# Kernel tuning notes

Hardware: AMD Instinct MI355X
Metric: run time of the kernel (lower is better)

## Reference

```python
import jax, jax.numpy as jnp
import numpy as np

N_WORD = 50000
N_DOC = 10000
E_WW = 800000
E_WD = 320000


def _sage(h_src, h_dst, src, dst, n_dst, W_self, W_neigh, b):
    # DGL SAGEConv('mean'): fc_self(h_dst) + fc_neigh(mean_{u in N(v)} h_u) + bias
    ones = jnp.ones((src.shape[0],), dtype=h_src.dtype)
    deg = jax.ops.segment_sum(ones, dst, num_segments=n_dst)            # [n_dst]
    agg = jax.ops.segment_sum(h_src[src], dst, num_segments=n_dst)      # [n_dst, d]
    mean = agg / jnp.maximum(deg, 1.0)[:, None]                          # zero for isolated
    return h_dst @ W_self + mean @ W_neigh + b


def _layer(xw, xd, edges, Ws, Wn, b):
    (ww_s, ww_d, wwr_s, wwr_d, wd_s, wd_d, wdr_s, wdr_d) = edges
    # relations targeting 'word': word2word, word2wordr, word2documentr
    h_ww = _sage(xw, xw, ww_s, ww_d, N_WORD, Ws[0], Wn[0], b[0])
    h_wwr = _sage(xw, xw, wwr_s, wwr_d, N_WORD, Ws[1], Wn[1], b[1])
    h_wdr = _sage(xd, xw, wdr_s, wdr_d, N_WORD, Ws[3], Wn[3], b[3])
    # relation targeting 'document': word2document
    h_wd = _sage(xw, xd, wd_s, wd_d, N_DOC, Ws[2], Wn[2], b[2])
    # HeteroGraphConv aggregate='stack' then torch.sum(dim=1) == sum over relations; then relu
    return jax.nn.relu(h_ww + h_wwr + h_wdr), jax.nn.relu(h_wd)


def setup_inputs() -> dict:
    key = jax.random.key(0)
    ks = jax.random.split(key, 20)
    d_in, d_h = 256, 128
    inp = {
        "x_word": jax.random.normal(ks[0], (N_WORD, d_in), jnp.float32),
        "x_doc": jax.random.normal(ks[1], (N_DOC, d_in), jnp.float32),
        "ww_src": jax.random.randint(ks[2], (E_WW,), 0, N_WORD, jnp.int32),
        "ww_dst": jax.random.randint(ks[3], (E_WW,), 0, N_WORD, jnp.int32),
        "wwr_src": jax.random.randint(ks[4], (E_WW,), 0, N_WORD, jnp.int32),
        "wwr_dst": jax.random.randint(ks[5], (E_WW,), 0, N_WORD, jnp.int32),
        "wd_src": jax.random.randint(ks[6], (E_WD,), 0, N_WORD, jnp.int32),
        "wd_dst": jax.random.randint(ks[7], (E_WD,), 0, N_DOC, jnp.int32),
        "wdr_src": jax.random.randint(ks[8], (E_WD,), 0, N_DOC, jnp.int32),
        "wdr_dst": jax.random.randint(ks[9], (E_WD,), 0, N_WORD, jnp.int32),
        "Wself1": jax.random.normal(ks[10], (4, d_in, d_h), jnp.float32) * (1.0 / np.sqrt(d_in)),
        "Wneigh1": jax.random.normal(ks[11], (4, d_in, d_h), jnp.float32) * (1.0 / np.sqrt(d_in)),
        "b1": jnp.zeros((4, d_h), jnp.float32),
        "Wself2": jax.random.normal(ks[12], (4, d_h, d_h), jnp.float32) * (1.0 / np.sqrt(d_h)),
        "Wneigh2": jax.random.normal(ks[13], (4, d_h, d_h), jnp.float32) * (1.0 / np.sqrt(d_h)),
        "b2": jnp.zeros((4, d_h), jnp.float32),
        "lin_w": jax.random.normal(ks[14], (1, d_h), jnp.float32) * (1.0 / np.sqrt(d_h)),
        "lin_b": jnp.ones((1,), jnp.float32),
    }
    return inp


def reference(x_word, x_doc, ww_src, ww_dst, wwr_src, wwr_dst, wd_src, wd_dst,
              wdr_src, wdr_dst, Wself1, Wneigh1, b1, Wself2, Wneigh2, b2, lin_w, lin_b):
    edges = (ww_src, ww_dst, wwr_src, wwr_dst, wd_src, wd_dst, wdr_src, wdr_dst)
    xw, xd = _layer(x_word, x_doc, edges, Wself1, Wneigh1, b1)
    xw, xd = _layer(xw, xd, edges, Wself2, Wneigh2, b2)
    out_w = jax.nn.sigmoid(xw @ lin_w.T + lin_b)  # [N_WORD, 1]
    out_d = jax.nn.sigmoid(xd @ lin_w.T + lin_b)  # [N_DOC, 1]
    return out_w, out_d
```

## Files before the change

kernel.cpp:

```cpp
#include <hip/hip_runtime.h>
#include <math.h>

#define N_WORD 50000
#define N_DOC  10000
#define E_WW   800000
#define E_WD   320000
#define D_IN   256
#define D_H    128

#define NPB    1024
#define NBK_W  49
#define NBK_D  10
#define BKT    (3 * NBK_W + NBK_D)
#define EPB    4096
#define NBLK_WW 196
#define NBLK_WD 79
#define NBLK_TOT (2 * NBLK_WW + 2 * NBLK_WD)
#define PACK_BLKS 145

#define CAP_WW  18432
#define CAP_WDR 8192
#define CAP_WD  34816

#define WSTRIP ((N_WORD + 63) / 64)
#define DSTRIP ((N_DOC + 63) / 64)
#define NSTRIP (WSTRIP + DSTRIP)

typedef __attribute__((ext_vector_type(8))) short short8;
typedef __attribute__((ext_vector_type(4))) float f32x4;

__device__ inline unsigned short f2bf(float f) {
  unsigned u = __float_as_uint(f);
  u = (u + 0x7fffu + ((u >> 16) & 1u)) >> 16;
  return (unsigned short)u;
}

struct G6 { const short* B[6]; unsigned short* C[6]; };

template <int ABF, int K>
__device__ void gemm_body(const void* __restrict__ Aw, const void* __restrict__ Ad,
                          const G6& g, int blk, short* As) {
  constexpr int kd8s = (K == 256) ? 5 : 4;
  constexpr int stride = K + 8;
  constexpr int kd8 = K >> 3;
  const void* A; int M, row0, h0, h1;
  if (blk < WSTRIP) { A = Aw; M = N_WORD; row0 = blk << 6; h0 = 0; h1 = 4; }
  else { A = Ad; M = N_DOC; row0 = (blk - WSTRIP) << 6; h0 = 4; h1 = 6; }
  constexpr int total = kd8 << 6;
  for (int c = threadIdx.x; c < total; c += 256) {
    int row = c >> kd8s;
    int col8 = c & (kd8 - 1);
    int grow = row0 + row; if (grow >= M) grow = M - 1;
    short8 v;
    if (ABF) {
      v = *(const short8*)((const short*)A + (size_t)grow * K + col8 * 8);
    } else {
      const float* a = (const float*)A + (size_t)grow * K + col8 * 8;
      float4 a0 = *(const float4*)a, a1 = *(const float4*)(a + 4);
      v[0] = (short)f2bf(a0.x); v[1] = (short)f2bf(a0.y);
      v[2] = (short)f2bf(a0.z); v[3] = (short)f2bf(a0.w);
      v[4] = (short)f2bf(a1.x); v[5] = (short)f2bf(a1.y);
      v[6] = (short)f2bf(a1.z); v[7] = (short)f2bf(a1.w);
    }
    *(short8*)&As[row * stride + col8 * 8] = v;
  }
  __syncthreads();
  int wid = threadIdx.x >> 6, lane = threadIdx.x & 63;
  int r = lane & 15, quad = lane >> 4;
  constexpr int KT = K >> 5;
  int m0 = row0 + wid * 16;
  for (int h = h0; h < h1; ++h) {
    const short* Bp = g.B[h];
    f32x4 acc[8];
#pragma unroll
    for (int nt = 0; nt < 8; ++nt) acc[nt] = (f32x4){0.f, 0.f, 0.f, 0.f};
    for (int kt = 0; kt < KT; ++kt) {
      short8 af = *(const short8*)&As[(wid * 16 + r) * stride + kt * 32 + quad * 8];
      const short* bbase = Bp + ((size_t)kt * 4096) + lane * 8;
#pragma unroll
      for (int nt = 0; nt < 8; ++nt) {
        short8 bf = *(const short8*)(bbase + (size_t)nt * 512);
        acc[nt] = __builtin_amdgcn_mfma_f32_16x16x32_bf16(af, bf, acc[nt], 0, 0, 0);
      }
    }
    unsigned short* C = g.C[h];
#pragma unroll
    for (int nt = 0; nt < 8; ++nt)
#pragma unroll
      for (int rr = 0; rr < 4; ++rr) {
        int row = m0 + quad * 4 + rr;
        if (row < M) C[(size_t)row * 128 + nt * 16 + r] = f2bf(acc[nt][rr]);
      }
  }
}

struct CSRB {
  const unsigned *st_ww, *st_wwr, *st_wdr, *st_wd;
  unsigned short *c_ww, *c_wwr, *c_wdr, *c_wd;
  int *rp_ww, *rp_wwr, *rp_wdr, *rp_wd;
  const int* bcnt;
};

__device__ void place_body(int g, const CSRB& q, char* smem) {
  int* cnt = (int*)smem;
  int* off = cnt + NPB;
  int* sm  = off + NPB;
  int* s_b = sm + 256;
  const unsigned* st; unsigned short* csr; int* rp; int relFirst, relLast, n, cap, Etot;
  if (g < NBK_W)            { st = q.st_ww;  csr = q.c_ww;  rp = q.rp_ww;  relFirst = 0;         relLast = NBK_W - 1;     n = N_WORD; cap = CAP_WW;  Etot = E_WW; }
  else if (g < 2 * NBK_W)   { st = q.st_wwr; csr = q.c_wwr; rp = q.rp_wwr; relFirst = NBK_W;     relLast = 2 * NBK_W - 1; n = N_WORD; cap = CAP_WW;  Etot = E_WW; }
  else if (g < 3 * NBK_W)   { st = q.st_wdr; csr = q.c_wdr; rp = q.rp_wdr; relFirst = 2 * NBK_W; relLast = 3 * NBK_W - 1; n = N_WORD; cap = CAP_WDR; Etot = E_WD; }
  else                      { st = q.st_wd;  csr = q.c_wd;  rp = q.rp_wd;  relFirst = 3 * NBK_W; relLast = BKT - 1;       n = N_DOC;  cap = CAP_WD;  Etot = E_WD; }
  int cb = g - relFirst;
  int tid = threadIdx.x;
  if (tid < 64) {
    int v = (tid < cb) ? q.bcnt[relFirst + tid] : 0;
#pragma unroll
    for (int o = 32; o > 0; o >>= 1) v += __shfl_xor(v, o);
    if (tid == 0) s_b[0] = v;
  }
  if (g == relLast && tid == 65) rp[n] = Etot;
  int node_base = cb << 10;
  int node_cnt = n - node_base; if (node_cnt > NPB) node_cnt = NPB;
  int ecnt = q.bcnt[g];
  const unsigned* w = st + (size_t)cb * cap;
  for (int i = tid; i < NPB; i += 256) cnt[i] = 0;
  __syncthreads();
  int bstart = s_b[0];
  for (int j = tid; j < ecnt; j += 256) atomicAdd(&cnt[w[j] >> 16], 1);
  __syncthreads();
  int c[4], s = 0;
#pragma unroll
  for (int jj = 0; jj < 4; ++jj) { c[jj] = cnt[tid * 4 + jj]; s += c[jj]; }
  sm[tid] = s;
  __syncthreads();
  for (int o = 1; o < 256; o <<= 1) {
    int add = (tid >= o) ? sm[tid - o] : 0;
    __syncthreads();
    sm[tid] += add;
    __syncthreads();
  }
  int ex = sm[tid] - s;
#pragma unroll
  for (int jj = 0; jj < 4; ++jj) { off[tid * 4 + jj] = ex; ex += c[jj]; }
  __syncthreads();
#pragma unroll
  for (int jj = 0; jj < 4; ++jj) {
    int i = tid * 4 + jj;
    if (i < node_cnt) rp[node_base + i] = bstart + off[i];
  }
  __syncthreads();
  for (int j = tid; j < ecnt; j += 256) {
    unsigned e = w[j];
    int p = atomicAdd(&off[e >> 16], 1);
    csr[bstart + p] = (unsigned short)(e & 0xFFFFu);
  }
}

__global__ __launch_bounds__(256) void gemm1_place(
    const float* __restrict__ Aw, const float* __restrict__ Ad, G6 g, CSRB q) {
  __shared__ char smem[64 * 264 * 2];
  if (blockIdx.x < NSTRIP) gemm_body<0, 256>(Aw, Ad, g, blockIdx.x, (short*)smem);
  else place_body(blockIdx.x - NSTRIP, q, smem);
}

__global__ __launch_bounds__(256) void gemm2_kernel(
    const void* __restrict__ Aw, const void* __restrict__ Ad, G6 g) {
  __shared__ short As[64 * 136];
  gemm_body<1, 128>(Aw, Ad, g, blockIdx.x, As);
}

__device__ inline void rel_map(int b, const int* wwd, const int* wwrd, const int* wdrd,
                               const int* wdd, const int*& dst, int& E, int& gbase, int& lb) {
  if (b < NBLK_WW) { dst = wwd; E = E_WW; gbase = 0; lb = b; }
  else if (b < 2 * NBLK_WW) { dst = wwrd; E = E_WW; gbase = NBK_W; lb = b - NBLK_WW; }
  else if (b < 2 * NBLK_WW + NBLK_WD) { dst = wdrd; E = E_WD; gbase = 2 * NBK_W; lb = b - 2 * NBLK_WW; }
  else { dst = wdd; E = E_WD; gbase = 3 * NBK_W; lb = b - 2 * NBLK_WW - NBLK_WD; }
}

__global__ __launch_bounds__(256) void binpack_kernel(
    const int* wws, const int* wwd, const int* wwrs, const int* wwrd,
    const int* wdrs, const int* wdrd, const int* wds, const int* wdd,
    int* bcnt, unsigned* st_ww, unsigned* st_wwr, unsigned* st_wdr, unsigned* st_wd,
    const float* __restrict__ Ws1, const float* __restrict__ Wn1,
    const float* __restrict__ Ws2, const float* __restrict__ Wn2,
    short* __restrict__ Bp1, short* __restrict__ Bp2,
    const float* __restrict__ b1, const float* __restrict__ b2,
    float* __restrict__ bs1, float* __restrict__ bs2) {
  int b = blockIdx.x;
  if (b >= NBLK_TOT) {
    int tid = (b - NBLK_TOT) * 256 + threadIdx.x;
    const int L1T = 6 * 4096;
    const int L2T = 6 * 2048;
    if (tid >= L1T + L2T) {
      int t = tid - (L1T + L2T);
      if (t < 128) bs1[t] = b1[t] + b1[128 + t] + b1[384 + t];
      else if (t < 256) { int u = t - 128; bs2[u] = b2[u] + b2[128 + u] + b2[384 + u]; }
      return;
    }
    const float *src0, *src1 = nullptr, *src2 = nullptr;
    short* dstp;
    int kt, nt, lane;
    if (tid < L1T) {
      int mat = tid / 4096, rem = tid % 4096;
      kt = rem / 512; nt = (rem / 64) % 8; lane = rem % 64;
      const int W1 = 256 * 128;
      if (mat == 0) { src0 = Ws1; src1 = Ws1 + W1; src2 = Ws1 + 3 * W1; }
      else if (mat <= 4) src0 = Wn1 + (size_t)(mat - 1) * W1;
      else src0 = Ws1 + 2 * W1;
      dstp = Bp1 + (size_t)mat * W1 + ((size_t)(kt * 8 + nt) * 64 + lane) * 8;
    } else {
      int t2 = tid - L1T;
      int mat = t2 / 2048, rem = t2 % 2048;
      kt = rem / 512; nt = (rem / 64) % 8; lane = rem % 64;
      const int W2 = 128 * 128;
      if (mat == 0) { src0 = Ws2; src1 = Ws2 + W2; src2 = Ws2 + 3 * W2; }
      else if (mat <= 4) src0 = Wn2 + (size_t)(mat - 1) * W2;
      else src0 = Ws2 + 2 * W2;
      dstp = Bp2 + (size_t)mat * W2 + ((size_t)(kt * 8 + nt) * 64 + lane) * 8;
    }
    int n = nt * 16 + (lane & 15);
    int kb = kt * 32 + (lane >> 4) * 8;
    short8 v;
#pragma unroll
    for (int j = 0; j < 8; ++j) {
      float f = src0[(size_t)(kb + j) * 128 + n];
      if (src1) f += src1[(size_t)(kb + j) * 128 + n] + src2[(size_t)(kb + j) * 128 + n];
      v[j] = (short)f2bf(f);
    }
    *(short8*)dstp = v;
    return;
  }
  __shared__ int h[4][64], wb[4][64], cur[4][64];
  const int* dst; int E, gbase, lb;
  rel_map(b, wwd, wwrd, wdrd, wdd, dst, E, gbase, lb);
  const int* src; unsigned* st; int cap;
  if (b < NBLK_WW) { src = wws; st = st_ww; cap = CAP_WW; }
  else if (b < 2 * NBLK_WW) { src = wwrs; st = st_wwr; cap = CAP_WW; }
  else if (b < 2 * NBLK_WW + NBLK_WD) { src = wdrs; st = st_wdr; cap = CAP_WDR; }
  else { src = wds; st = st_wd; cap = CAP_WD; }
  int tid = threadIdx.x;
  int wave = tid >> 6;
  ((int*)h)[tid] = 0;
  ((int*)cur)[tid] = 0;
  __syncthreads();
  int e0 = lb * EPB;
#pragma unroll
  for (int k = 0; k < EPB / 256; ++k) {
    int i = e0 + k * 256 + tid;
    if (i < E) atomicAdd(&h[wave][dst[i] >> 10], 1);
  }
  __syncthreads();
  if (tid < NBK_W) {
    int t0 = h[0][tid], t1 = h[1][tid], t2 = h[2][tid], t3 = h[3][tid];
    int tot = t0 + t1 + t2 + t3;
    int base = tot ? atomicAdd(&bcnt[gbase + tid], tot) : 0;
    wb[0][tid] = base;
    wb[1][tid] = base + t0;
    wb[2][tid] = base + t0 + t1;
    wb[3][tid] = base + t0 + t1 + t2;
  }
  __syncthreads();
#pragma unroll
  for (int k = 0; k < EPB / 256; ++k) {
    int i = e0 + k * 256 + tid;
    if (i < E) {
      int d = dst[i];
      int bk = d >> 10;
      int l = atomicAdd(&cur[wave][bk], 1);
      st[(size_t)bk * cap + wb[wave][bk] + l] =
          (unsigned)(src[i] & 0xFFFF) | ((unsigned)(d & (NPB - 1)) << 16);
    }
  }
}

__device__ inline void accum_rel(const unsigned* __restrict__ y,
                                 const unsigned short* __restrict__ csr,
                                 int beg, int end, int lane, float& f0, float& f1) {
  float a0 = 0.f, a1 = 0.f;
  for (int base = beg; base < end; base += 64) {
    int cnt = end - base; if (cnt > 64) cnt = 64;
    int ld = base + lane; if (ld >= end) ld = end - 1;
    int idx = csr[ld];
    int j = 0;
    for (; j + 7 < cnt; j += 8) {
      unsigned u[8];
#pragma unroll
      for (int k = 0; k < 8; ++k) {
        int s = __builtin_amdgcn_readlane(idx, j + k);
        u[k] = y[((size_t)s << 6) + lane];
      }
#pragma unroll
      for (int k = 0; k < 8; ++k) {
        a0 += __uint_as_float(u[k] << 16);
        a1 += __uint_as_float(u[k] & 0xffff0000u);
      }
    }
    for (; j < cnt; ++j) {
      int s = __builtin_amdgcn_readlane(idx, j);
      unsigned uu = y[((size_t)s << 6) + lane];
      a0 += __uint_as_float(uu << 16);
      a1 += __uint_as_float(uu & 0xffff0000u);
    }
  }
  int deg = end - beg;
  float inv = 1.0f / (float)(deg > 1 ? deg : 1);
  f0 += a0 * inv;
  f1 += a1 * inv;
}

__global__ __launch_bounds__(256) void gather_all(
    const unsigned* __restrict__ y_ww, const unsigned* __restrict__ y_wwr,
    const unsigned* __restrict__ y_wdr, const unsigned* __restrict__ y_wd,
    const unsigned short* __restrict__ c_ww, const unsigned short* __restrict__ c_wwr,
    const unsigned short* __restrict__ c_wdr, const unsigned short* __restrict__ c_wd,
    const int* __restrict__ r_ww, const int* __restrict__ r_wwr,
    const int* __restrict__ r_wdr, const int* __restrict__ r_wd,
    const unsigned* __restrict__ tW, const unsigned* __restrict__ tD,
    const float* __restrict__ bW, const float* __restrict__ bD,
    const float* __restrict__ lw, const float* __restrict__ lb,
    unsigned* __restrict__ oW16, unsigned* __restrict__ oD16,
    float* __restrict__ oF, int mode) {
  int gn = (blockIdx.x << 2) + (threadIdx.x >> 6);
  if (gn >= N_WORD + N_DOC) return;
  int lane = threadIdx.x & 63;
  float f0, f1;
  if (gn < N_WORD) {
    int node = gn;
    unsigned tu = tW[((size_t)node << 6) + lane];
    f0 = __uint_as_float(tu << 16);
    f1 = __uint_as_float(tu & 0xffff0000u);
    accum_rel(y_ww, c_ww, r_ww[node], r_ww[node + 1], lane, f0, f1);
    accum_rel(y_wwr, c_wwr, r_wwr[node], r_wwr[node + 1], lane, f0, f1);
    accum_rel(y_wdr, c_wdr, r_wdr[node], r_wdr[node + 1], lane, f0, f1);
    float2 bv = ((const float2*)bW)[lane];
    f0 = fmaxf(f0 + bv.x, 0.f);
    f1 = fmaxf(f1 + bv.y, 0.f);
    if (mode == 1) {
      oW16[((size_t)node << 6) + lane] = (unsigned)f2bf(f0) | ((unsigned)f2bf(f1) << 16);
    } else {
      float2 lv = ((const float2*)lw)[lane];
      float s = f0 * lv.x + f1 * lv.y;
#pragma unroll
      for (int off = 32; off > 0; off >>= 1) s += __shfl_xor(s, off);
      if (lane == 0) oF[node] = 1.0f / (1.0f + expf(-(s + lb[0])));
    }
  } else {
    int node = gn - N_WORD;
    unsigned tu = tD[((size_t)node << 6) + lane];
    f0 = __uint_as_float(tu << 16);
    f1 = __uint_as_float(tu & 0xffff0000u);
    accum_rel(y_wd, c_wd, r_wd[node], r_wd[node + 1], lane, f0, f1);
    float2 bv = ((const float2*)bD)[lane];
    f0 = fmaxf(f0 + bv.x, 0.f);
    f1 = fmaxf(f1 + bv.y, 0.f);
    if (mode == 1) {
      oD16[((size_t)node << 6) + lane] = (unsigned)f2bf(f0) | ((unsigned)f2bf(f1) << 16);
    } else {
      float2 lv = ((const float2*)lw)[lane];
      float s = f0 * lv.x + f1 * lv.y;
#pragma unroll
      for (int off = 32; off > 0; off >>= 1) s += __shfl_xor(s, off);
      if (lane == 0) oF[N_WORD + node] = 1.0f / (1.0f + expf(-(s + lb[0])));
    }
  }
}

extern "C" void kernel_launch(void* const* d_in, const int* in_sizes, int n_in,
                              void* d_out, int out_size, void* d_ws, size_t ws_size,
                              hipStream_t stream) {
  const float* xw      = (const float*)d_in[0];
  const float* xd      = (const float*)d_in[1];
  const int*   ww_src  = (const int*)d_in[2];
  const int*   ww_dst  = (const int*)d_in[3];
  const int*   wwr_src = (const int*)d_in[4];
  const int*   wwr_dst = (const int*)d_in[5];
  const int*   wd_src  = (const int*)d_in[6];
  const int*   wd_dst  = (const int*)d_in[7];
  const int*   wdr_src = (const int*)d_in[8];
  const int*   wdr_dst = (const int*)d_in[9];
  const float* Ws1     = (const float*)d_in[10];
  const float* Wn1     = (const float*)d_in[11];
  const float* b1      = (const float*)d_in[12];
  const float* Ws2     = (const float*)d_in[13];
  const float* Wn2     = (const float*)d_in[14];
  const float* b2      = (const float*)d_in[15];
  const float* lin_w   = (const float*)d_in[16];
  const float* lin_b   = (const float*)d_in[17];
  float* out = (float*)d_out;

  char* p = (char*)d_ws;
  auto alloc = [&](size_t nbytes) {
    char* r = p;
    p += (nbytes + 255) & ~(size_t)255;
    return r;
  };
  unsigned* twA  = (unsigned*)alloc((size_t)N_WORD * D_H * 2);
  unsigned* tdA  = (unsigned*)alloc((size_t)N_DOC * D_H * 2);
  unsigned* xw1B = (unsigned*)alloc((size_t)N_WORD * D_H * 2);
  unsigned* xd1B = (unsigned*)alloc((size_t)N_DOC * D_H * 2);
  unsigned* yB0 = (unsigned*)alloc((size_t)N_WORD * D_H * 2);
  unsigned* yB1 = (unsigned*)alloc((size_t)N_WORD * D_H * 2);
  unsigned* yB2 = (unsigned*)alloc((size_t)N_WORD * D_H * 2);
  unsigned* ydB = (unsigned*)alloc((size_t)N_DOC * D_H * 2);
  unsigned short* csr_ww  = (unsigned short*)alloc((size_t)E_WW * 2);
  unsigned short* csr_wwr = (unsigned short*)alloc((size_t)E_WW * 2);
  unsigned short* csr_wdr = (unsigned short*)alloc((size_t)E_WD * 2);
  unsigned short* csr_wd  = (unsigned short*)alloc((size_t)E_WD * 2);
  int* rp_ww  = (int*)alloc((size_t)(N_WORD + 1) * 4);
  int* rp_wwr = (int*)alloc((size_t)(N_WORD + 1) * 4);
  int* rp_wdr = (int*)alloc((size_t)(N_WORD + 1) * 4);
  int* rp_wd  = (int*)alloc((size_t)(N_DOC + 1) * 4);
  short* Bp1 = (short*)alloc((size_t)6 * 256 * 128 * 2);
  short* Bp2 = (short*)alloc((size_t)6 * 128 * 128 * 2);
  int* bcnt  = (int*)alloc((size_t)BKT * 4);
  float* bs1 = (float*)alloc(D_H * 4);
  float* bs2 = (float*)alloc(D_H * 4);
  unsigned* st_ww  = yB0;
  unsigned* st_wwr = st_ww + (size_t)NBK_W * CAP_WW;
  unsigned* st_wdr = yB1;
  unsigned* st_wd  = st_wdr + (size_t)NBK_W * CAP_WDR;

  hipMemsetAsync(bcnt, 0, BKT * 4, stream);
  binpack_kernel<<<NBLK_TOT + PACK_BLKS, 256, 0, stream>>>(
      ww_src, ww_dst, wwr_src, wwr_dst, wdr_src, wdr_dst, wd_src, wd_dst,
      bcnt, st_ww, st_wwr, st_wdr, st_wd,
      Ws1, Wn1, Ws2, Wn2, Bp1, Bp2, b1, b2, bs1, bs2);

  const int W1 = 256 * 128;
  const int W2 = 128 * 128;

  G6 g1;
  g1.B[0] = Bp1 + 0 * W1; g1.C[0] = (unsigned short*)twA;
  g1.B[1] = Bp1 + 1 * W1; g1.C[1] = (unsigned short*)yB0;
  g1.B[2] = Bp1 + 2 * W1; g1.C[2] = (unsigned short*)yB1;
  g1.B[3] = Bp1 + 3 * W1; g1.C[3] = (unsigned short*)yB2;
  g1.B[4] = Bp1 + 5 * W1; g1.C[4] = (unsigned short*)tdA;
  g1.B[5] = Bp1 + 4 * W1; g1.C[5] = (unsigned short*)ydB;
  CSRB q;
  q.st_ww = st_ww; q.st_wwr = st_wwr; q.st_wdr = st_wdr; q.st_wd = st_wd;
  q.c_ww = csr_ww; q.c_wwr = csr_wwr; q.c_wdr = csr_wdr; q.c_wd = csr_wd;
  q.rp_ww = rp_ww; q.rp_wwr = rp_wwr; q.rp_wdr = rp_wdr; q.rp_wd = rp_wd;
  q.bcnt = bcnt;
  g1.C[1] = (unsigned short*)yB2;
  g1.C[2] = (unsigned short*)xw1B;
  g1.C[3] = (unsigned short*)twA;
  (void)0;
  static_assert(true, "");
  unsigned* yBX = (unsigned*)alloc((size_t)N_WORD * D_H * 2);
  g1.C[0] = (unsigned short*)twA;
  g1.C[1] = (unsigned short*)yB2;
  g1.C[2] = (unsigned short*)xw1B;
  g1.C[3] = (unsigned short*)yBX;
  g1.C[4] = (unsigned short*)tdA;
  g1.C[5] = (unsigned short*)ydB;
  gemm1_place<<<NSTRIP + BKT, 256, 0, stream>>>(xw, xd, g1, q);
  gather_all<<<(N_WORD + N_DOC + 3) / 4, 256, 0, stream>>>(
      yB2, xw1B, ydB, yBX, csr_ww, csr_wwr, csr_wdr, csr_wd,
      rp_ww, rp_wwr, rp_wdr, rp_wd, twA, tdA, bs1, b1 + 256,
      lin_w, lin_b, yB0, xd1B, nullptr, 1);

  G6 g2;
  g2.B[0] = Bp2 + 0 * W2; g2.C[0] = (unsigned short*)twA;
  g2.B[1] = Bp2 + 1 * W2; g2.C[1] = (unsigned short*)yB2;
  g2.B[2] = Bp2 + 2 * W2; g2.C[2] = (unsigned short*)xw1B;
  g2.B[3] = Bp2 + 3 * W2; g2.C[3] = (unsigned short*)yBX;
  g2.B[4] = Bp2 + 5 * W2; g2.C[4] = (unsigned short*)tdA;
  g2.B[5] = Bp2 + 4 * W2; g2.C[5] = (unsigned short*)ydB;
  gemm2_kernel<<<NSTRIP, 256, 0, stream>>>(yB0, xd1B, g2);
  gather_all<<<(N_WORD + N_DOC + 3) / 4, 256, 0, stream>>>(
      yB2, xw1B, ydB, yBX, csr_ww, csr_wwr, csr_wdr, csr_wd,
      rp_ww, rp_wwr, rp_wdr, rp_wd, twA, tdA, bs2, b2 + 256,
      lin_w, lin_b, nullptr, nullptr, out, 2);
}
```

Before: 443.2 us.

## Load GEMM A fragments straight into registers and schedule place blocks first

After: 428.7 us. -3.3%, faster.

```diff
diff --git a/kernel.cpp b/kernel.cpp
--- a/kernel.cpp
+++ b/kernel.cpp
@@ -39,48 +39,46 @@
 
 template <int ABF, int K>
 __device__ void gemm_body(const void* __restrict__ Aw, const void* __restrict__ Ad,
-                          const G6& g, int blk, short* As) {
-  constexpr int kd8s = (K == 256) ? 5 : 4;
-  constexpr int stride = K + 8;
-  constexpr int kd8 = K >> 3;
+                          const G6& g, int blk) {
+  constexpr int KT = K >> 5;
+  int wid = threadIdx.x >> 6, lane = threadIdx.x & 63;
   const void* A; int M, row0, h0, h1;
   if (blk < WSTRIP) { A = Aw; M = N_WORD; row0 = blk << 6; h0 = 0; h1 = 4; }
   else { A = Ad; M = N_DOC; row0 = (blk - WSTRIP) << 6; h0 = 4; h1 = 6; }
-  constexpr int total = kd8 << 6;
-  for (int c = threadIdx.x; c < total; c += 256) {
-    int row = c >> kd8s;
-    int col8 = c & (kd8 - 1);
-    int grow = row0 + row; if (grow >= M) grow = M - 1;
-    short8 v;
-    if (ABF) {
-      v = *(const short8*)((const short*)A + (size_t)grow * K + col8 * 8);
-    } else {
-      const float* a = (const float*)A + (size_t)grow * K + col8 * 8;
-      float4 a0 = *(const float4*)a, a1 = *(const float4*)(a + 4);
+  int r = lane & 15, quad = lane >> 4;
+  int m0 = row0 + wid * 16;
+  int mA = m0 + r; if (mA >= M) mA = M - 1;
+  short8 afr[KT];
+  if (ABF) {
+    const short* ap = (const short*)A + (size_t)mA * K + quad * 8;
+#pragma unroll
+    for (int kt = 0; kt < KT; ++kt) afr[kt] = *(const short8*)(ap + kt * 32);
+  } else {
+    const float* ap = (const float*)A + (size_t)mA * K + quad * 8;
+#pragma unroll
+    for (int kt = 0; kt < KT; ++kt) {
+      float4 a0 = *(const float4*)(ap + kt * 32);
+      float4 a1 = *(const float4*)(ap + kt * 32 + 4);
+      short8 v;
       v[0] = (short)f2bf(a0.x); v[1] = (short)f2bf(a0.y);
       v[2] = (short)f2bf(a0.z); v[3] = (short)f2bf(a0.w);
       v[4] = (short)f2bf(a1.x); v[5] = (short)f2bf(a1.y);
       v[6] = (short)f2bf(a1.z); v[7] = (short)f2bf(a1.w);
-    }
-    *(short8*)&As[row * stride + col8 * 8] = v;
-  }
-  __syncthreads();
-  int wid = threadIdx.x >> 6, lane = threadIdx.x & 63;
-  int r = lane & 15, quad = lane >> 4;
-  constexpr int KT = K >> 5;
-  int m0 = row0 + wid * 16;
+      afr[kt] = v;
+    }
+  }
   for (int h = h0; h < h1; ++h) {
     const short* Bp = g.B[h];
     f32x4 acc[8];
 #pragma unroll
     for (int nt = 0; nt < 8; ++nt) acc[nt] = (f32x4){0.f, 0.f, 0.f, 0.f};
+#pragma unroll
     for (int kt = 0; kt < KT; ++kt) {
-      short8 af = *(const short8*)&As[(wid * 16 + r) * stride + kt * 32 + quad * 8];
       const short* bbase = Bp + ((size_t)kt * 4096) + lane * 8;
 #pragma unroll
       for (int nt = 0; nt < 8; ++nt) {
         short8 bf = *(const short8*)(bbase + (size_t)nt * 512);
-        acc[nt] = __builtin_amdgcn_mfma_f32_16x16x32_bf16(af, bf, acc[nt], 0, 0, 0);
+        acc[nt] = __builtin_amdgcn_mfma_f32_16x16x32_bf16(afr[kt], bf, acc[nt], 0, 0, 0);
       }
     }
     unsigned short* C = g.C[h];
@@ -101,8 +99,8 @@
   const int* bcnt;
 };
 
-__device__ void place_body(int g, const CSRB& q, char* smem) {
-  int* cnt = (int*)smem;
+__device__ void place_body(int g, const CSRB& q, int* smem) {
+  int* cnt = smem;
   int* off = cnt + NPB;
   int* sm  = off + NPB;
   int* s_b = sm + 256;
@@ -157,17 +155,16 @@
   }
 }
 
-__global__ __launch_bounds__(256) void gemm1_place(
+__global__ __launch_bounds__(256, 4) void gemm1_place(
     const float* __restrict__ Aw, const float* __restrict__ Ad, G6 g, CSRB q) {
-  __shared__ char smem[64 * 264 * 2];
-  if (blockIdx.x < NSTRIP) gemm_body<0, 256>(Aw, Ad, g, blockIdx.x, (short*)smem);
-  else place_body(blockIdx.x - NSTRIP, q, smem);
-}
-
-__global__ __launch_bounds__(256) void gemm2_kernel(
+  __shared__ int smem[NPB * 2 + 256 + 1];
+  if (blockIdx.x < BKT) place_body(blockIdx.x, q, smem);
+  else gemm_body<0, 256>(Aw, Ad, g, blockIdx.x - BKT);
+}
+
+__global__ __launch_bounds__(256, 4) void gemm2_kernel(
     const void* __restrict__ Aw, const void* __restrict__ Ad, G6 g) {
-  __shared__ short As[64 * 136];
-  gemm_body<1, 128>(Aw, Ad, g, blockIdx.x, As);
+  gemm_body<1, 128>(Aw, Ad, g, blockIdx.x);
 }
 
 __device__ inline void rel_map(int b, const int* wwd, const int* wwrd, const int* wdrd,
@@ -416,6 +413,7 @@
   int* bcnt  = (int*)alloc((size_t)BKT * 4);
   float* bs1 = (float*)alloc(D_H * 4);
   float* bs2 = (float*)alloc(D_H * 4);
+  unsigned* yBX = (unsigned*)alloc((size_t)N_WORD * D_H * 2);
   unsigned* st_ww  = yB0;
   unsigned* st_wwr = st_ww + (size_t)NBK_W * CAP_WW;
   unsigned* st_wdr = yB1;
@@ -432,9 +430,9 @@
 
   G6 g1;
   g1.B[0] = Bp1 + 0 * W1; g1.C[0] = (unsigned short*)twA;
-  g1.B[1] = Bp1 + 1 * W1; g1.C[1] = (unsigned short*)yB0;
-  g1.B[2] = Bp1 + 2 * W1; g1.C[2] = (unsigned short*)yB1;
-  g1.B[3] = Bp1 + 3 * W1; g1.C[3] = (unsigned short*)yB2;
+  g1.B[1] = Bp1 + 1 * W1; g1.C[1] = (unsigned short*)yB2;
+  g1.B[2] = Bp1 + 2 * W1; g1.C[2] = (unsigned short*)xw1B;
+  g1.B[3] = Bp1 + 3 * W1; g1.C[3] = (unsigned short*)yBX;
   g1.B[4] = Bp1 + 5 * W1; g1.C[4] = (unsigned short*)tdA;
   g1.B[5] = Bp1 + 4 * W1; g1.C[5] = (unsigned short*)ydB;
   CSRB q;
@@ -442,19 +440,7 @@
   q.c_ww = csr_ww; q.c_wwr = csr_wwr; q.c_wdr = csr_wdr; q.c_wd = csr_wd;
   q.rp_ww = rp_ww; q.rp_wwr = rp_wwr; q.rp_wdr = rp_wdr; q.rp_wd = rp_wd;
   q.bcnt = bcnt;
-  g1.C[1] = (unsigned short*)yB2;
-  g1.C[2] = (unsigned short*)xw1B;
-  g1.C[3] = (unsigned short*)twA;
-  (void)0;
-  static_assert(true, "");
-  unsigned* yBX = (unsigned*)alloc((size_t)N_WORD * D_H * 2);
-  g1.C[0] = (unsigned short*)twA;
-  g1.C[1] = (unsigned short*)yB2;
-  g1.C[2] = (unsigned short*)xw1B;
-  g1.C[3] = (unsigned short*)yBX;
-  g1.C[4] = (unsigned short*)tdA;
-  g1.C[5] = (unsigned short*)ydB;
-  gemm1_place<<<NSTRIP + BKT, 256, 0, stream>>>(xw, xd, g1, q);
+  gemm1_place<<<BKT + NSTRIP, 256, 0, stream>>>(xw, xd, g1, q);
   gather_all<<<(N_WORD + N_DOC + 3) / 4, 256, 0, stream>>>(
       yB2, xw1B, ydB, yBX, csr_ww, csr_wwr, csr_wdr, csr_wd,
       rp_ww, rp_wwr, rp_wdr, rp_wd, twA, tdA, bs1, b1 + 256,
```
